# Kernel optimization log

Hardware: AMD Instinct MI355X
Metric: run time of the kernel (lower is better)

## Reference

```python
import jax, jax.numpy as jnp
import numpy as np

ALPHA = 0.2
NEG_INF = -9e15


def setup_inputs() -> dict:
    key = jax.random.key(0)
    k1, k2, k3, k4 = jax.random.split(key, 4)
    N, F_IN, F_OUT, H = 4096, 1, 64, 12
    x = jax.random.normal(k1, (N, F_IN), dtype=jnp.float32)
    adj = jax.random.randint(k2, (N, N), 0, 2).astype(jnp.int32)
    # per-head params stacked: W [H, F_IN, F_OUT], a [H, 2*F_OUT, 1]
    W = jax.random.normal(k3, (H, F_IN, F_OUT), dtype=jnp.float32) * 0.1
    a = jax.random.normal(k4, (H, 2 * F_OUT, 1), dtype=jnp.float32) * 0.1
    return {"x": x, "adj": adj, "W": W, "a": a}


def reference(x, adj, W, a):
    # h per head: [H, N, F_OUT]
    h = jnp.einsum('nf,hfo->hno', x, W)
    F_out = h.shape[-1]
    # a_input[i,j] = concat(h_i, h_j), so a_input @ a = h_i.a_src + h_j.a_dst
    a_src = a[:, :F_out, 0]   # [H, F_OUT]
    a_dst = a[:, F_out:, 0]   # [H, F_OUT]
    e_src = jnp.einsum('hnf,hf->hn', h, a_src)  # [H, N]
    e_dst = jnp.einsum('hnf,hf->hn', h, a_dst)  # [H, N]
    e = jax.nn.leaky_relu(e_src[:, :, None] + e_dst[:, None, :], ALPHA)  # [H,N,N]
    e = jnp.where(adj[None] > 0, e, NEG_INF)
    attn = jax.nn.softmax(e, axis=-1)           # softmax over neighbors j
    h_prime = jnp.einsum('hij,hjf->hif', attn, h)  # [H, N, F_OUT]
    # concat heads along feature dim -> [N, H*F_OUT]
    N = h_prime.shape[1]
    return jnp.transpose(h_prime, (1, 0, 2)).reshape(N, -1)
```

## Files before the change

### kernel.cpp

```cpp
#include <hip/hip_runtime.h>

#define GAT_H 12
#define GAT_N 4096
#define GAT_F 64
#define LOG2E 1.4426950408889634f


__device__ float g_tab2[GAT_H * GAT_N];
__device__ float g_sd[2 * GAT_H + 1];

__global__ __launch_bounds__(256) void gat_prep(const float* __restrict__ W,
                                                const float* __restrict__ a,
                                                const float* __restrict__ x) {
    const int b    = blockIdx.x;
    const int tid  = threadIdx.x;
    const int lane = tid & 63;
    const int wave = tid >> 6;

    if (b < GAT_H) {
        if (wave == 0) {
            const float wf = W[b * GAT_F + lane];
            float ps = wf * a[b * 2 * GAT_F + lane];
            float pd = wf * a[b * 2 * GAT_F + GAT_F + lane];
            #pragma unroll
            for (int off = 32; off > 0; off >>= 1) {
                ps += __shfl_xor(ps, off, 64);
                pd += __shfl_xor(pd, off, 64);
            }
            if (lane == 0) { g_sd[b] = ps; g_sd[GAT_H + b] = pd; }
        }
        return;
    }
    if (b == GAT_H) {
        if (wave == 0) {
            float s = 0.0f;
            #pragma unroll
            for (int j = 0; j < GAT_N / 64; ++j) s += x[j * 64 + lane];
            #pragma unroll
            for (int off = 32; off > 0; off >>= 1) s += __shfl_xor(s, off, 64);
            if (lane == 0) g_sd[2 * GAT_H] = s * (1.0f / GAT_N);
        }
        return;
    }

    const int bt    = b - (GAT_H + 1);
    const int h     = bt >> 2;
    const int chunk = bt & 3;
    const float wf  = W[h * GAT_F + lane];
    float pd = wf * a[h * 2 * GAT_F + GAT_F + lane];
    #pragma unroll
    for (int off = 32; off > 0; off >>= 1) pd += __shfl_xor(pd, off, 64);
    const float dl5 = 0.2f * pd * LOG2E;
    #pragma unroll
    for (int k = 0; k < 4; ++k) {
        const int j = chunk * 1024 + k * 256 + tid;
        g_tab2[h * GAT_N + j] = __builtin_amdgcn_exp2f(dl5 * x[j]);
    }
}

__global__ __launch_bounds__(512) void gat_main(const float* __restrict__ x,
                                                const int* __restrict__ adj,
                                                const float* __restrict__ W,
                                                float* __restrict__ out) {
    __shared__ float tab_lds[2][GAT_H][256];
    __shared__ float cbuf[4][GAT_H];

    const int tid   = threadIdx.x;
    const int row0  = blockIdx.x * 4;
    const int lane  = tid & 63;
    const int wave  = tid >> 6;
    const int r     = wave >> 1;
    const int hg    = wave & 1;
    const int hbase = hg * 6;
    const int row   = row0 + r;

    const float xrow = x[row];
    float rho[6];
    #pragma unroll
    for (int hh = 0; hh < 6; ++hh)
        rho[hh] = __uint_as_float(__builtin_amdgcn_readfirstlane(__float_as_uint(
            __builtin_amdgcn_exp2f(-0.8f * LOG2E * xrow * g_sd[hbase + hh]))));

    float den[6], num[6];
    #pragma unroll
    for (int hh = 0; hh < 6; ++hh) { den[hh] = 0.0f; num[hh] = 0.0f; }

    const float2* __restrict__ tg = (const float2*)g_tab2;
    int sh[3], sj[3];
    #pragma unroll
    for (int k = 0; k < 3; ++k) {
        const int p = k * 512 + tid;
        sh[k] = p >> 7;
        sj[k] = p & 127;
    }
    float2* __restrict__ lds2 = (float2*)tab_lds;

    #pragma unroll
    for (int k = 0; k < 3; ++k)
        lds2[sh[k] * 128 + sj[k]] = tg[sh[k] * (GAT_N / 2) + sj[k]];
    const int4*   __restrict__ a4p = (const int4*)(adj + (size_t)row * GAT_N);
    const float4* __restrict__ x4  = (const float4*)x;
    int4   a_c = a4p[lane];
    float4 x_c = x4[lane];
    __syncthreads();

    #pragma unroll 2
    for (int it = 0; it < 16; ++it) {
        const int buf = it & 1;
        const int nit = (it < 15) ? it + 1 : 15;

        float2 st[3];
        #pragma unroll
        for (int k = 0; k < 3; ++k)
            st[k] = tg[sh[k] * (GAT_N / 2) + nit * 128 + sj[k]];
        const int ni = nit * 64 + lane;
        const int4   a_n = a4p[ni];
        const float4 x_n = x4[ni];

        const int*   ai = (const int*)&a_c;
        const float* xp = (const float*)&x_c;
        float am[4], axj[4];
        #pragma unroll
        for (int e = 0; e < 4; ++e) {
            am[e]  = (float)ai[e];
            axj[e] = am[e] * xp[e];
        }

        #pragma unroll
        for (int hh = 0; hh < 6; ++hh) {
            const float4 e2v = *(const float4*)&tab_lds[buf][hbase + hh][4 * lane];
            const float* e2  = (const float*)&e2v;
            #pragma unroll
            for (int e = 0; e < 4; ++e) {
                const float w  = e2[e] * e2[e];
                const float w4 = w * w;
                const float p  = fmaxf(w4, rho[hh]) * e2[e];
                den[hh] = fmaf(p, am[e],  den[hh]);
                num[hh] = fmaf(p, axj[e], num[hh]);
            }
        }

        #pragma unroll
        for (int k = 0; k < 3; ++k)
            lds2[(buf ^ 1) * (GAT_H * 128) + sh[k] * 128 + sj[k]] = st[k];
        a_c = a_n; x_c = x_n;
        __syncthreads();
    }

    #pragma unroll
    for (int hh = 0; hh < 6; ++hh) {
        #pragma unroll
        for (int off = 32; off > 0; off >>= 1) {
            den[hh] += __shfl_xor(den[hh], off, 64);
            num[hh] += __shfl_xor(num[hh], off, 64);
        }
    }
    if (lane == 0) {
        const float fb = g_sd[2 * GAT_H];
        #pragma unroll
        for (int hh = 0; hh < 6; ++hh)
            cbuf[r][hbase + hh] = den[hh] > 0.0f ? num[hh] / den[hh] : fb;
    }
    __syncthreads();

    #pragma unroll
    for (int rr = 0; rr < 4; ++rr) {
        const size_t base = (size_t)(row0 + rr) * (GAT_H * GAT_F);
        #pragma unroll
        for (int k = 0; k < 2; ++k) {
            const int pos = k * 512 + tid;
            if (pos < GAT_H * GAT_F)
                out[base + pos] = cbuf[rr][pos >> 6] * W[pos];
        }
    }
}

extern "C" void kernel_launch(void* const* d_in, const int* in_sizes, int n_in,
                              void* d_out, int out_size, void* d_ws, size_t ws_size,
                              hipStream_t stream) {
    const float* x   = (const float*)d_in[0];
    const int*   adj = (const int*)d_in[1];
    const float* W   = (const float*)d_in[2];
    const float* a   = (const float*)d_in[3];
    float* out = (float*)d_out;
    (void)d_ws; (void)ws_size;

    gat_prep<<<GAT_H + 1 + 48, 256, 0, stream>>>(W, a, x);
    gat_main<<<GAT_N / 4, 512, 0, stream>>>(x, adj, W, out);
}
```

Measured before the change: 135.4 us.

## Process two rows per wave and deepen adjacency prefetch to two iterations

```diff
diff --git a/kernel.cpp b/kernel.cpp
--- a/kernel.cpp
+++ b/kernel.cpp
@@ -63,27 +63,33 @@
                                                 const float* __restrict__ W,
                                                 float* __restrict__ out) {
     __shared__ float tab_lds[2][GAT_H][256];
-    __shared__ float cbuf[4][GAT_H];
+    __shared__ float cbuf[8][GAT_H];
 
     const int tid   = threadIdx.x;
-    const int row0  = blockIdx.x * 4;
+    const int row0  = blockIdx.x * 8;
     const int lane  = tid & 63;
     const int wave  = tid >> 6;
-    const int r     = wave >> 1;
+    const int rp    = wave >> 1;
     const int hg    = wave & 1;
     const int hbase = hg * 6;
-    const int row   = row0 + r;
-
-    const float xrow = x[row];
-    float rho[6];
-    #pragma unroll
-    for (int hh = 0; hh < 6; ++hh)
-        rho[hh] = __uint_as_float(__builtin_amdgcn_readfirstlane(__float_as_uint(
-            __builtin_amdgcn_exp2f(-0.8f * LOG2E * xrow * g_sd[hbase + hh]))));
-
-    float den[6], num[6];
-    #pragma unroll
-    for (int hh = 0; hh < 6; ++hh) { den[hh] = 0.0f; num[hh] = 0.0f; }
+    const int rowA  = row0 + rp * 2;
+
+    float rho[2][6];
+    #pragma unroll
+    for (int r = 0; r < 2; ++r) {
+        const float xr = x[rowA + r];
+        #pragma unroll
+        for (int hh = 0; hh < 6; ++hh)
+            rho[r][hh] = __uint_as_float(__builtin_amdgcn_readfirstlane(
+                __float_as_uint(__builtin_amdgcn_exp2f(
+                    -0.8f * LOG2E * xr * g_sd[hbase + hh]))));
+    }
+
+    float den[2][6], num[2][6];
+    #pragma unroll
+    for (int r = 0; r < 2; ++r)
+        #pragma unroll
+        for (int hh = 0; hh < 6; ++hh) { den[r][hh] = 0.0f; num[r][hh] = 0.0f; }
 
     const float2* __restrict__ tg = (const float2*)g_tab2;
     int sh[3], sj[3];
@@ -98,33 +104,44 @@
     #pragma unroll
     for (int k = 0; k < 3; ++k)
         lds2[sh[k] * 128 + sj[k]] = tg[sh[k] * (GAT_N / 2) + sj[k]];
-    const int4*   __restrict__ a4p = (const int4*)(adj + (size_t)row * GAT_N);
-    const float4* __restrict__ x4  = (const float4*)x;
-    int4   a_c = a4p[lane];
-    float4 x_c = x4[lane];
+    const int4*   __restrict__ a4p0 = (const int4*)(adj + (size_t)rowA * GAT_N);
+    const int4*   __restrict__ a4p1 = a4p0 + (GAT_N / 4);
+    const float4* __restrict__ x4   = (const float4*)x;
+
+    int4   aP0[2], aP1[2];
+    float4 xP[2];
+    aP0[0] = a4p0[lane];      aP1[0] = a4p1[lane];      xP[0] = x4[lane];
+    aP0[1] = a4p0[64 + lane]; aP1[1] = a4p1[64 + lane]; xP[1] = x4[64 + lane];
     __syncthreads();
 
     #pragma unroll 2
     for (int it = 0; it < 16; ++it) {
         const int buf = it & 1;
-        const int nit = (it < 15) ? it + 1 : 15;
-
+
+        float am[2][4], axj[2][4];
+        {
+            const int*   ai0 = (const int*)&aP0[buf];
+            const int*   ai1 = (const int*)&aP1[buf];
+            const float* xp  = (const float*)&xP[buf];
+            #pragma unroll
+            for (int e = 0; e < 4; ++e) {
+                am[0][e]  = (float)ai0[e];
+                am[1][e]  = (float)ai1[e];
+                axj[0][e] = am[0][e] * xp[e];
+                axj[1][e] = am[1][e] * xp[e];
+            }
+        }
+
+        const int n1 = (it < 15) ? it + 1 : 15;
         float2 st[3];
         #pragma unroll
         for (int k = 0; k < 3; ++k)
-            st[k] = tg[sh[k] * (GAT_N / 2) + nit * 128 + sj[k]];
-        const int ni = nit * 64 + lane;
-        const int4   a_n = a4p[ni];
-        const float4 x_n = x4[ni];
-
-        const int*   ai = (const int*)&a_c;
-        const float* xp = (const float*)&x_c;
-        float am[4], axj[4];
-        #pragma unroll
-        for (int e = 0; e < 4; ++e) {
-            am[e]  = (float)ai[e];
-            axj[e] = am[e] * xp[e];
-        }
+            st[k] = tg[sh[k] * (GAT_N / 2) + n1 * 128 + sj[k]];
+
+        const int n2i = ((it < 14) ? it + 2 : 15) * 64 + lane;
+        aP0[buf] = a4p0[n2i];
+        aP1[buf] = a4p1[n2i];
+        xP[buf]  = x4[n2i];
 
         #pragma unroll
         for (int hh = 0; hh < 6; ++hh) {
@@ -134,37 +151,40 @@
             for (int e = 0; e < 4; ++e) {
                 const float w  = e2[e] * e2[e];
                 const float w4 = w * w;
-                const float p  = fmaxf(w4, rho[hh]) * e2[e];
-                den[hh] = fmaf(p, am[e],  den[hh]);
-                num[hh] = fmaf(p, axj[e], num[hh]);
+                const float p0 = fmaxf(w4, rho[0][hh]) * e2[e];
+                const float p1 = fmaxf(w4, rho[1][hh]) * e2[e];
+                den[0][hh] = fmaf(p0, am[0][e],  den[0][hh]);
+                num[0][hh] = fmaf(p0, axj[0][e], num[0][hh]);
+                den[1][hh] = fmaf(p1, am[1][e],  den[1][hh]);
+                num[1][hh] = fmaf(p1, axj[1][e], num[1][hh]);
             }
         }
 
         #pragma unroll
         for (int k = 0; k < 3; ++k)
             lds2[(buf ^ 1) * (GAT_H * 128) + sh[k] * 128 + sj[k]] = st[k];
-        a_c = a_n; x_c = x_n;
         __syncthreads();
     }
 
     #pragma unroll
-    for (int hh = 0; hh < 6; ++hh) {
-        #pragma unroll
-        for (int off = 32; off > 0; off >>= 1) {
-            den[hh] += __shfl_xor(den[hh], off, 64);
-            num[hh] += __shfl_xor(num[hh], off, 64);
-        }
-    }
-    if (lane == 0) {
-        const float fb = g_sd[2 * GAT_H];
-        #pragma unroll
-        for (int hh = 0; hh < 6; ++hh)
-            cbuf[r][hbase + hh] = den[hh] > 0.0f ? num[hh] / den[hh] : fb;
+    for (int r = 0; r < 2; ++r) {
+        #pragma unroll
+        for (int hh = 0; hh < 6; ++hh) {
+            float d = den[r][hh], n = num[r][hh];
+            #pragma unroll
+            for (int off = 32; off > 0; off >>= 1) {
+                d += __shfl_xor(d, off, 64);
+                n += __shfl_xor(n, off, 64);
+            }
+            if (lane == 0)
+                cbuf[rp * 2 + r][hbase + hh] =
+                    d > 0.0f ? n / d : g_sd[2 * GAT_H];
+        }
     }
     __syncthreads();
 
     #pragma unroll
-    for (int rr = 0; rr < 4; ++rr) {
+    for (int rr = 0; rr < 8; ++rr) {
         const size_t base = (size_t)(row0 + rr) * (GAT_H * GAT_F);
         #pragma unroll
         for (int k = 0; k < 2; ++k) {
@@ -186,5 +206,5 @@
     (void)d_ws; (void)ws_size;
 
     gat_prep<<<GAT_H + 1 + 48, 256, 0, stream>>>(W, a, x);
-    gat_main<<<GAT_N / 4, 512, 0, stream>>>(x, adj, W, out);
+    gat_main<<<GAT_N / 8, 512, 0, stream>>>(x, adj, W, out);
 }
```

After: 128.8 us. 4.9% less time.
